# Performance work log

Measured on AMD Instinct MI355X. Metric: run time of the kernel, lower is better.

The kernel has to match this reference:

```python
import jax, jax.numpy as jnp
import numpy as np

N = 30000      # nodes
E = 300000     # edges (before self-loops)
G = 1024       # graphs
D_IN = 256     # embedding dim
HID = 256      # hidden dim
H = 8          # heads
C = HID // H   # per-head dim
VOCAB = 65


def setup_inputs() -> dict:
    key = jax.random.key(0)
    ks = jax.random.split(key, 32)
    inp = {
        "x_ids": jax.random.randint(ks[0], (N,), 0, VOCAB),
        "edge_index": jax.random.randint(ks[1], (2, E), 0, N),
        "batch_ids": (jnp.arange(N) * G) // N,  # sorted graph ids, every graph non-empty
        "emb": jax.random.normal(ks[2], (VOCAB, D_IN)) * 0.05,
        "fw": jax.random.normal(ks[3], (1, HID)) * 0.05,
        "fb": jnp.zeros((1,)),
    }
    k = 4
    for i, d_in in enumerate([D_IN, HID, HID, HID, HID], start=1):
        inp[f"W{i}"] = jax.random.normal(ks[k], (HID, d_in)) * (1.0 / np.sqrt(d_in)); k += 1
        inp[f"as{i}"] = jax.random.normal(ks[k], (H, C)) * 0.1; k += 1
        inp[f"ad{i}"] = jax.random.normal(ks[k], (H, C)) * 0.1; k += 1
        inp[f"b{i}"] = jnp.zeros((HID,))
    return inp


def _gat_conv(x, src, dst, W, a_src, a_dst, b):
    # x: [N, d_in] -> h: [N, H, C]
    h = (x @ W.T).reshape(N, H, C)
    e_src = jnp.einsum("nhc,hc->nh", h, a_src)  # [N, H]
    e_dst = jnp.einsum("nhc,hc->nh", h, a_dst)
    e = jax.nn.leaky_relu(e_src[src] + e_dst[dst], 0.2)  # [E', H]
    m = jax.ops.segment_max(e, dst, num_segments=N)      # segment softmax over incoming edges
    ex = jnp.exp(e - m[dst])
    s = jax.ops.segment_sum(ex, dst, num_segments=N)
    alpha = ex / (s[dst] + 1e-16)                        # [E', H]
    out = jax.ops.segment_sum(h[src] * alpha[:, :, None], dst, num_segments=N)
    return out.reshape(N, H * C) + b


def reference(x_ids, edge_index, batch_ids, emb,
              W1, as1, ad1, b1, W2, as2, ad2, b2, W3, as3, ad3, b3,
              W4, as4, ad4, b4, W5, as5, ad5, b5, fw, fb):
    # Embedding with max_norm=1: rescale looked-up rows whose L2 norm exceeds 1
    x = emb[x_ids]
    nrm = jnp.linalg.norm(x, axis=-1, keepdims=True)
    x = x * jnp.minimum(1.0, 1.0 / (nrm + 1e-12))
    # add self-loops once (PyG GATConv default)
    loop = jnp.arange(N)
    src = jnp.concatenate([edge_index[0], loop])
    dst = jnp.concatenate([edge_index[1], loop])
    x = jax.nn.relu(_gat_conv(x, src, dst, W1, as1, ad1, b1))
    x = jax.nn.relu(_gat_conv(x, src, dst, W2, as2, ad2, b2))
    x = jax.nn.relu(_gat_conv(x, src, dst, W3, as3, ad3, b3))
    x = jax.nn.relu(_gat_conv(x, src, dst, W4, as4, ad4, b4))
    x = jax.nn.relu(_gat_conv(x, src, dst, W5, as5, ad5, b5))
    pooled = jax.ops.segment_max(x, batch_ids, num_segments=G)  # [G, HID]
    return (pooled @ fw.T + fb).reshape(-1)  # [G]
```

## Files before the change

kernel.cpp:

```cpp
#include <hip/hip_runtime.h>
#include <float.h>
#include <math.h>

constexpr int NN  = 30000;
constexpr int EE  = 300000;
constexpr int GG  = 1024;
constexpr int HID = 256;
constexpr int NH  = 8;
constexpr int EP  = EE + NN;
constexpr int NP  = 30080;

typedef short bf16x8 __attribute__((ext_vector_type(8)));
typedef float f32x4 __attribute__((ext_vector_type(4)));

__device__ __forceinline__ void gload_lds16(const void* g, void* l) {
    __builtin_amdgcn_global_load_lds(
        (const __attribute__((address_space(1))) unsigned int*)g,
        (__attribute__((address_space(3))) unsigned int*)l, 16, 0, 0);
}

__device__ __forceinline__ void f2hilo(float x, unsigned short& h, unsigned short& l) {
    unsigned u = __float_as_uint(x);
    h = (unsigned short)(u >> 16);
    float hv = __uint_as_float(u & 0xFFFF0000u);
    float r = x - hv;
    unsigned v = __float_as_uint(r);
    unsigned rnd = ((v >> 16) & 1u) + 0x7FFFu;
    l = (unsigned short)((v + rnd) >> 16);
}

__device__ __forceinline__ float bf2f(unsigned short u) {
    return __uint_as_float(((unsigned)u) << 16);
}

__global__ void k_hist(const int* __restrict__ edst, int* __restrict__ cnt) {
    int i = blockIdx.x * blockDim.x + threadIdx.x;
    if (i >= EP) return;
    int d = (i < EE) ? edst[i] : (i - EE);
    atomicAdd(&cnt[d], 1);
}

__global__ void k_scan(const int* __restrict__ cnt, int* __restrict__ indptr) {
    __shared__ int wtot[16];
    __shared__ int carry_s;
    int tid = threadIdx.x;
    int lane = tid & 63, wid = tid >> 6;
    if (tid == 0) carry_s = 0;
    __syncthreads();
    for (int base = 0; base < NN; base += 1024) {
        int i = base + tid;
        int v = (i < NN) ? cnt[i] : 0;
        int incl = v;
        #pragma unroll
        for (int off = 1; off < 64; off <<= 1) {
            int t = __shfl_up(incl, off, 64);
            if (lane >= off) incl += t;
        }
        if (lane == 63) wtot[wid] = incl;
        __syncthreads();
        int wpre = 0;
        for (int w = 0; w < wid; ++w) wpre += wtot[w];
        int c = carry_s;
        if (i < NN) indptr[i] = c + wpre + incl - v;
        int tot = 0;
        for (int w = 0; w < 16; ++w) tot += wtot[w];
        __syncthreads();
        if (tid == 0) carry_s = c + tot;
        __syncthreads();
    }
    if (tid == 0) indptr[NN] = carry_s;
}

__global__ void k_fill(const int* __restrict__ esrc, const int* __restrict__ edst,
                       const int* __restrict__ indptr, int* __restrict__ cursor,
                       int* __restrict__ srcs) {
    int i = blockIdx.x * blockDim.x + threadIdx.x;
    if (i >= EP) return;
    int d, s;
    if (i < EE) { d = edst[i]; s = esrc[i]; } else { d = i - EE; s = i - EE; }
    int pos = indptr[d] + atomicAdd(&cursor[d], 1);
    srcs[pos] = s;
}

__global__ void k_sortseg(int* __restrict__ srcs, const int* __restrict__ indptr) {
    int node = blockIdx.x * blockDim.x + threadIdx.x;
    if (node >= NN) return;
    int b = indptr[node], e = indptr[node + 1];
    for (int i = b + 1; i < e; ++i) {
        int v = srcs[i];
        int j = i - 1;
        while (j >= b && srcs[j] > v) { srcs[j + 1] = srcs[j]; --j; }
        srcs[j + 1] = v;
    }
}

__global__ void k_starts(const int* __restrict__ batch, int* __restrict__ starts) {
    int i = blockIdx.x * blockDim.x + threadIdx.x;
    if (i >= NN) return;
    int b = batch[i];
    if (i == 0 || batch[i - 1] != b) starts[b] = i;
    if (i == NN - 1) starts[GG] = NN;
}

__global__ void k_wconv(const float* __restrict__ W1, const float* __restrict__ W2,
                        const float* __restrict__ W3, const float* __restrict__ W4,
                        const float* __restrict__ W5,
                        unsigned short* __restrict__ Whi, unsigned short* __restrict__ Wlo) {
    int i = blockIdx.x * blockDim.x + threadIdx.x;
    int l = blockIdx.y;
    const float* W = (l == 0) ? W1 : (l == 1) ? W2 : (l == 2) ? W3 : (l == 3) ? W4 : W5;
    unsigned short h, lo;
    f2hilo(W[i], h, lo);
    Whi[(size_t)l * 65536 + i] = h;
    Wlo[(size_t)l * 65536 + i] = lo;
}

__global__ void k_wtilde(const float* __restrict__ W, const float* __restrict__ as,
                         const float* __restrict__ ad,
                         unsigned short* __restrict__ Wthi, unsigned short* __restrict__ Wtlo) {
    int t = blockIdx.x;
    int k = threadIdx.x;
    int h = t >> 1, type = t & 1;
    const float* a = type ? ad : as;
    float v = 0.f;
    for (int c = 0; c < 32; ++c)
        v = fmaf(a[h * 32 + c], W[(size_t)(h * 32 + c) * HID + k], v);
    unsigned short hi, lo;
    f2hilo(v, hi, lo);
    Wthi[t * 256 + k] = hi;
    Wtlo[t * 256 + k] = lo;
}

__global__ void k_embed(const int* __restrict__ ids, const float* __restrict__ emb,
                        unsigned short* __restrict__ Phi, unsigned short* __restrict__ Plo) {
    int w = (blockIdx.x * blockDim.x + threadIdx.x) >> 6;
    if (w >= NN) return;
    int lane = threadIdx.x & 63;
    const float4 v = *(const float4*)(emb + (size_t)ids[w] * HID + lane * 4);
    float ss = v.x * v.x + v.y * v.y + v.z * v.z + v.w * v.w;
    #pragma unroll
    for (int off = 32; off >= 1; off >>= 1) ss += __shfl_xor(ss, off, 64);
    float nrm = sqrtf(ss);
    float sc = fminf(1.0f, 1.0f / (nrm + 1e-12f));
    float o[4] = {v.x * sc, v.y * sc, v.z * sc, v.w * sc};
    ushort4 hv, lv;
    f2hilo(o[0], hv.x, lv.x); f2hilo(o[1], hv.y, lv.y);
    f2hilo(o[2], hv.z, lv.z); f2hilo(o[3], hv.w, lv.w);
    *(ushort4*)(Phi + (size_t)w * HID + lane * 4) = hv;
    *(ushort4*)(Plo + (size_t)w * HID + lane * 4) = lv;
}

__global__ __launch_bounds__(256) void k_gemm(const unsigned short* __restrict__ Ahi,
                                              const unsigned short* __restrict__ Alo,
                                              const unsigned short* __restrict__ Bhi,
                                              const unsigned short* __restrict__ Blo,
                                              const unsigned short* __restrict__ Wthi,
                                              const unsigned short* __restrict__ Wtlo,
                                              float* __restrict__ O,
                                              float* __restrict__ es,
                                              float* __restrict__ ed, int M) {
    __shared__ unsigned short lds[4][128 * 64];
    const int tid = threadIdx.x;
    const int m0 = blockIdx.x * 128;
    const int n0 = blockIdx.y * 128;
    const int wid = tid >> 6, lane = tid & 63;
    const int wm = wid >> 1, wn = wid & 1;
    const int r16 = lane & 15, kq = lane >> 4;
    const bool doScore = (blockIdx.y == 1);

    f32x4 acc[4][4];
    f32x4 acc_s[4];
    #pragma unroll
    for (int i = 0; i < 4; ++i) {
        acc_s[i] = (f32x4){0.f, 0.f, 0.f, 0.f};
        #pragma unroll
        for (int j = 0; j < 4; ++j) acc[i][j] = (f32x4){0.f, 0.f, 0.f, 0.f};
    }

    for (int kt = 0; kt < 4; ++kt) {
        const int kk = kt * 64;
        #pragma unroll
        for (int rnd = 0; rnd < 4; ++rnd) {
            int q = rnd * 256 + tid;
            int row = q >> 3, c = q & 7;
            int sc = c ^ (row & 7);
            size_t goffA = (size_t)(m0 + row) * HID + kk + sc * 8;
            size_t goffB = (size_t)(n0 + row) * HID + kk + sc * 8;
            gload_lds16(Ahi + goffA, &lds[0][q * 8]);
            gload_lds16(Alo + goffA, &lds[1][q * 8]);
            gload_lds16(Bhi + goffB, &lds[2][q * 8]);
            gload_lds16(Blo + goffB, &lds[3][q * 8]);
        }
        __syncthreads();
        #pragma unroll
        for (int ks = 0; ks < 2; ++ks) {
            bf16x8 ah[4], al[4], bh[4], bl[4];
            #pragma unroll
            for (int f = 0; f < 4; ++f) {
                int rowa = wm * 64 + f * 16 + r16;
                int ca = (ks * 4 + kq) ^ (rowa & 7);
                int offa = rowa * 64 + ca * 8;
                ah[f] = *(const bf16x8*)&lds[0][offa];
                al[f] = *(const bf16x8*)&lds[1][offa];
                int rowb = wn * 64 + f * 16 + r16;
                int cb = (ks * 4 + kq) ^ (rowb & 7);
                int offb = rowb * 64 + cb * 8;
                bh[f] = *(const bf16x8*)&lds[2][offb];
                bl[f] = *(const bf16x8*)&lds[3][offb];
            }
            #pragma unroll
            for (int mi = 0; mi < 4; ++mi)
                #pragma unroll
                for (int ni = 0; ni < 4; ++ni) {
                    acc[mi][ni] = __builtin_amdgcn_mfma_f32_16x16x32_bf16(ah[mi], bh[ni], acc[mi][ni], 0, 0, 0);
                    acc[mi][ni] = __builtin_amdgcn_mfma_f32_16x16x32_bf16(ah[mi], bl[ni], acc[mi][ni], 0, 0, 0);
                    acc[mi][ni] = __builtin_amdgcn_mfma_f32_16x16x32_bf16(al[mi], bh[ni], acc[mi][ni], 0, 0, 0);
                }
            if (doScore && wn == ks) {
                const size_t wtoff = (size_t)r16 * HID + kk + ks * 32 + kq * 8;
                bf16x8 wth = *(const bf16x8*)(Wthi + wtoff);
                bf16x8 wtl = *(const bf16x8*)(Wtlo + wtoff);
                #pragma unroll
                for (int mi = 0; mi < 4; ++mi) {
                    acc_s[mi] = __builtin_amdgcn_mfma_f32_16x16x32_bf16(ah[mi], wth, acc_s[mi], 0, 0, 0);
                    acc_s[mi] = __builtin_amdgcn_mfma_f32_16x16x32_bf16(ah[mi], wtl, acc_s[mi], 0, 0, 0);
                    acc_s[mi] = __builtin_amdgcn_mfma_f32_16x16x32_bf16(al[mi], wth, acc_s[mi], 0, 0, 0);
                }
            }
        }
        __syncthreads();
    }
    #pragma unroll
    for (int mi = 0; mi < 4; ++mi) {
        #pragma unroll
        for (int q = 0; q < 4; ++q) {
            int row = m0 + wm * 64 + mi * 16 + kq * 4 + q;
            if (row < M) {
                #pragma unroll
                for (int ni = 0; ni < 4; ++ni)
                    O[(size_t)row * HID + n0 + wn * 64 + ni * 16 + r16] = acc[mi][ni][q];
            }
        }
    }
    if (doScore) {
        float* sl = (float*)&lds[0][0];
        if (wn == 1) {
            #pragma unroll
            for (int mi = 0; mi < 4; ++mi)
                *(f32x4*)&sl[((wm * 4 + mi) * 64 + lane) * 4] = acc_s[mi];
        }
        __syncthreads();
        if (wn == 0) {
            #pragma unroll
            for (int mi = 0; mi < 4; ++mi) {
                f32x4 o = *(const f32x4*)&sl[((wm * 4 + mi) * 64 + lane) * 4];
                o += acc_s[mi];
                int h = r16 >> 1;
                #pragma unroll
                for (int q = 0; q < 4; ++q) {
                    int row = m0 + wm * 64 + mi * 16 + kq * 4 + q;
                    if (row < M) {
                        if ((r16 & 1) == 0) es[row * NH + h] = o[q];
                        else               ed[row * NH + h] = o[q];
                    }
                }
            }
        }
    }
}

__global__ __launch_bounds__(256) void k_aggregate(const float* __restrict__ H,
                                                   const float* __restrict__ es,
                                                   const float* __restrict__ ed,
                                                   const int* __restrict__ indptr,
                                                   const int* __restrict__ srcs,
                                                   const float* __restrict__ bias,
                                                   unsigned short* __restrict__ Phi,
                                                   unsigned short* __restrict__ Plo) {
    int node = (blockIdx.x * blockDim.x + threadIdx.x) >> 6;
    if (node >= NN) return;
    int lane = threadIdx.x & 63;
    int head = lane >> 3;
    int b0 = indptr[node], e0 = indptr[node + 1];
    float edv = ed[node * NH + head];
    float4 a[4];
    float s[4];
    #pragma unroll
    for (int u = 0; u < 4; ++u) { a[u] = (float4){0.f, 0.f, 0.f, 0.f}; s[u] = 0.f; }
    int j = b0;
    for (; j + 3 < e0; j += 4) {
        #pragma unroll
        for (int u = 0; u < 4; ++u) {
            int x = srcs[j + u];
            float e = es[x * NH + head] + edv;
            e = (e > 0.f) ? e : 0.2f * e;
            float4 hv = *(const float4*)(H + (size_t)x * HID + lane * 4);
            float w = expf(e);
            s[u] += w;
            a[u].x = fmaf(w, hv.x, a[u].x); a[u].y = fmaf(w, hv.y, a[u].y);
            a[u].z = fmaf(w, hv.z, a[u].z); a[u].w = fmaf(w, hv.w, a[u].w);
        }
    }
    for (; j < e0; ++j) {
        int x = srcs[j];
        float e = es[x * NH + head] + edv;
        e = (e > 0.f) ? e : 0.2f * e;
        float4 hv = *(const float4*)(H + (size_t)x * HID + lane * 4);
        float w = expf(e);
        s[0] += w;
        a[0].x = fmaf(w, hv.x, a[0].x); a[0].y = fmaf(w, hv.y, a[0].y);
        a[0].z = fmaf(w, hv.z, a[0].z); a[0].w = fmaf(w, hv.w, a[0].w);
    }
    float sum = (s[0] + s[1]) + (s[2] + s[3]);
    float ax = (a[0].x + a[1].x) + (a[2].x + a[3].x);
    float ay = (a[0].y + a[1].y) + (a[2].y + a[3].y);
    float az = (a[0].z + a[1].z) + (a[2].z + a[3].z);
    float aw = (a[0].w + a[1].w) + (a[2].w + a[3].w);
    float inv = 1.f / (sum + 1e-16f);
    float4 bv = *(const float4*)(bias + lane * 4);
    float o[4];
    o[0] = fmaxf(fmaf(ax, inv, bv.x), 0.f);
    o[1] = fmaxf(fmaf(ay, inv, bv.y), 0.f);
    o[2] = fmaxf(fmaf(az, inv, bv.z), 0.f);
    o[3] = fmaxf(fmaf(aw, inv, bv.w), 0.f);
    ushort4 hv, lv;
    f2hilo(o[0], hv.x, lv.x); f2hilo(o[1], hv.y, lv.y);
    f2hilo(o[2], hv.z, lv.z); f2hilo(o[3], hv.w, lv.w);
    *(ushort4*)(Phi + (size_t)node * HID + lane * 4) = hv;
    *(ushort4*)(Plo + (size_t)node * HID + lane * 4) = lv;
}

__global__ void k_pool(const unsigned short* __restrict__ Phi,
                       const unsigned short* __restrict__ Plo,
                       const int* __restrict__ starts,
                       const float* __restrict__ fw, const float* __restrict__ fb,
                       float* __restrict__ out) {
    int g = (blockIdx.x * blockDim.x + threadIdx.x) >> 6;
    if (g >= GG) return;
    int lane = threadIdx.x & 63;
    int s = starts[g], e = starts[g + 1];
    float mx0 = -FLT_MAX, mx1 = -FLT_MAX, mx2 = -FLT_MAX, mx3 = -FLT_MAX;
    for (int n = s; n < e; ++n) {
        ushort4 hv = *(const ushort4*)(Phi + (size_t)n * HID + lane * 4);
        ushort4 lv = *(const ushort4*)(Plo + (size_t)n * HID + lane * 4);
        mx0 = fmaxf(mx0, bf2f(hv.x) + bf2f(lv.x));
        mx1 = fmaxf(mx1, bf2f(hv.y) + bf2f(lv.y));
        mx2 = fmaxf(mx2, bf2f(hv.z) + bf2f(lv.z));
        mx3 = fmaxf(mx3, bf2f(hv.w) + bf2f(lv.w));
    }
    float4 w = *(const float4*)(fw + lane * 4);
    float t = mx0 * w.x + mx1 * w.y + mx2 * w.z + mx3 * w.w;
    #pragma unroll
    for (int off = 32; off >= 1; off >>= 1) t += __shfl_xor(t, off, 64);
    if (lane == 0) out[g] = t + fb[0];
}

extern "C" void kernel_launch(void* const* d_in, const int* in_sizes, int n_in,
                              void* d_out, int out_size, void* d_ws, size_t ws_size,
                              hipStream_t stream) {
    const int* x_ids = (const int*)d_in[0];
    const int* eidx  = (const int*)d_in[1];
    const int* batch = (const int*)d_in[2];
    const float* emb = (const float*)d_in[3];
    const float* fw  = (const float*)d_in[4];
    const float* fb  = (const float*)d_in[5];
    const float* Wl[5], *asl[5], *adl[5], *bl[5];
    for (int l = 0; l < 5; ++l) {
        Wl[l]  = (const float*)d_in[6 + 4 * l];
        asl[l] = (const float*)d_in[7 + 4 * l];
        adl[l] = (const float*)d_in[8 + 4 * l];
        bl[l]  = (const float*)d_in[9 + 4 * l];
    }

    char* ws = (char*)d_ws;
    size_t off = 0;
    auto alloc = [&](size_t bytes) {
        void* p = ws + off;
        off = (off + bytes + 255) & ~(size_t)255;
        return p;
    };
    unsigned short* Phi  = (unsigned short*)alloc((size_t)NP * HID * 2);
    unsigned short* Plo  = (unsigned short*)alloc((size_t)NP * HID * 2);
    float* Q     = (float*)alloc((size_t)NN * HID * 4);
    unsigned short* Whi  = (unsigned short*)alloc((size_t)5 * HID * HID * 2);
    unsigned short* Wlo  = (unsigned short*)alloc((size_t)5 * HID * HID * 2);
    unsigned short* Wthi = (unsigned short*)alloc((size_t)5 * 16 * HID * 2);
    unsigned short* Wtlo = (unsigned short*)alloc((size_t)5 * 16 * HID * 2);
    float* es    = (float*)alloc((size_t)NN * NH * 4);
    float* ed    = (float*)alloc((size_t)NN * NH * 4);
    int* cnt     = (int*)alloc((size_t)NN * 4);
    int* cursor  = (int*)alloc((size_t)NN * 4);
    int* indptr  = (int*)alloc((size_t)(NN + 1) * 4);
    int* srcs    = (int*)alloc((size_t)EP * 4);
    int* starts  = (int*)alloc((size_t)(GG + 1) * 4);
    (void)ws_size; (void)in_sizes; (void)n_in; (void)out_size;

    hipMemsetAsync(cnt, 0, (size_t)NN * 4, stream);
    hipMemsetAsync(cursor, 0, (size_t)NN * 4, stream);

    k_hist<<<(EP + 255) / 256, 256, 0, stream>>>(eidx + EE, cnt);
    k_scan<<<1, 1024, 0, stream>>>(cnt, indptr);
    k_fill<<<(EP + 255) / 256, 256, 0, stream>>>(eidx, eidx + EE, indptr, cursor, srcs);
    k_sortseg<<<(NN + 255) / 256, 256, 0, stream>>>(srcs, indptr);
    k_starts<<<(NN + 255) / 256, 256, 0, stream>>>(batch, starts);
    k_wconv<<<dim3(HID * HID / 256, 5), 256, 0, stream>>>(Wl[0], Wl[1], Wl[2], Wl[3], Wl[4], Whi, Wlo);
    for (int l = 0; l < 5; ++l)
        k_wtilde<<<16, 256, 0, stream>>>(Wl[l], asl[l], adl[l],
                                         Wthi + (size_t)l * 16 * HID,
                                         Wtlo + (size_t)l * 16 * HID);
    k_embed<<<NN / 4, 256, 0, stream>>>(x_ids, emb, Phi, Plo);

    for (int l = 0; l < 5; ++l) {
        dim3 gg(NP / 128, HID / 128);
        k_gemm<<<gg, 256, 0, stream>>>(Phi, Plo,
                                       Whi + (size_t)l * HID * HID,
                                       Wlo + (size_t)l * HID * HID,
                                       Wthi + (size_t)l * 16 * HID,
                                       Wtlo + (size_t)l * 16 * HID,
                                       Q, es, ed, NN);
        k_aggregate<<<NN / 4, 256, 0, stream>>>(Q, es, ed, indptr, srcs, bl[l], Phi, Plo);
    }
    k_pool<<<GG / 4, 256, 0, stream>>>(Phi, Plo, starts, fw, fb, (float*)d_out);
}
```

Measured before the change: 527.8 us.

## Parallelize CSR scan, halve GEMM K-tile, split score MFMAs, deepen aggregation prefetch

Replaces the single-block serial prefix scan with a three-kernel block-parallel scan (block sums, offsets, per-block scan). The GEMM K-tile shrinks from 64 to 32 with a new LDS swizzle, which halves LDS use for higher occupancy but doubles the number of barriers. The attention-score MFMAs are now split across the two N-warps by M fragment, which removes the LDS reduction and its extra barrier. The aggregation loop is unrolled to 8 edges with all index, score and feature loads issued before the math, to get more gathers in flight at the cost of more registers.

```diff
diff --git a/kernel.cpp b/kernel.cpp
--- a/kernel.cpp
+++ b/kernel.cpp
@@ -9,6 +9,7 @@
 constexpr int NH  = 8;
 constexpr int EP  = EE + NN;
 constexpr int NP  = 30080;
+constexpr int NB  = (NN + 255) / 256;
 
 typedef short bf16x8 __attribute__((ext_vector_type(8)));
 typedef float f32x4 __attribute__((ext_vector_type(4)));
@@ -40,35 +41,53 @@
     atomicAdd(&cnt[d], 1);
 }
 
-__global__ void k_scan(const int* __restrict__ cnt, int* __restrict__ indptr) {
-    __shared__ int wtot[16];
-    __shared__ int carry_s;
-    int tid = threadIdx.x;
-    int lane = tid & 63, wid = tid >> 6;
-    if (tid == 0) carry_s = 0;
+__global__ void k_scan1(const int* __restrict__ cnt, int* __restrict__ bsum) {
+    int tid = threadIdx.x, lane = tid & 63, wid = tid >> 6;
+    int i = blockIdx.x * 256 + tid;
+    int v = (i < NN) ? cnt[i] : 0;
+    #pragma unroll
+    for (int off = 32; off >= 1; off >>= 1) v += __shfl_xor(v, off, 64);
+    __shared__ int ws[4];
+    if (lane == 0) ws[wid] = v;
     __syncthreads();
-    for (int base = 0; base < NN; base += 1024) {
-        int i = base + tid;
-        int v = (i < NN) ? cnt[i] : 0;
-        int incl = v;
-        #pragma unroll
-        for (int off = 1; off < 64; off <<= 1) {
-            int t = __shfl_up(incl, off, 64);
-            if (lane >= off) incl += t;
-        }
-        if (lane == 63) wtot[wid] = incl;
-        __syncthreads();
-        int wpre = 0;
-        for (int w = 0; w < wid; ++w) wpre += wtot[w];
-        int c = carry_s;
-        if (i < NN) indptr[i] = c + wpre + incl - v;
-        int tot = 0;
-        for (int w = 0; w < 16; ++w) tot += wtot[w];
-        __syncthreads();
-        if (tid == 0) carry_s = c + tot;
-        __syncthreads();
-    }
-    if (tid == 0) indptr[NN] = carry_s;
+    if (tid == 0) bsum[blockIdx.x] = ws[0] + ws[1] + ws[2] + ws[3];
+}
+
+__global__ void k_scan2(const int* __restrict__ bsum, int* __restrict__ boff,
+                        int* __restrict__ indptr) {
+    int tid = threadIdx.x, lane = tid & 63, wid = tid >> 6;
+    int v = (tid < NB) ? bsum[tid] : 0;
+    int incl = v;
+    #pragma unroll
+    for (int off = 1; off < 64; off <<= 1) {
+        int t = __shfl_up(incl, off, 64);
+        if (lane >= off) incl += t;
+    }
+    __shared__ int ws[2];
+    if (lane == 63) ws[wid] = incl;
+    __syncthreads();
+    int pre = (wid == 1) ? ws[0] : 0;
+    if (tid < NB) boff[tid] = pre + incl - v;
+    if (tid == 0) indptr[NN] = ws[0] + ws[1];
+}
+
+__global__ void k_scan3(const int* __restrict__ cnt, const int* __restrict__ boff,
+                        int* __restrict__ indptr) {
+    int tid = threadIdx.x, lane = tid & 63, wid = tid >> 6;
+    int i = blockIdx.x * 256 + tid;
+    int v = (i < NN) ? cnt[i] : 0;
+    int incl = v;
+    #pragma unroll
+    for (int off = 1; off < 64; off <<= 1) {
+        int t = __shfl_up(incl, off, 64);
+        if (lane >= off) incl += t;
+    }
+    __shared__ int ws[4];
+    if (lane == 63) ws[wid] = incl;
+    __syncthreads();
+    int pre = 0;
+    for (int w = 0; w < wid; ++w) pre += ws[w];
+    if (i < NN) indptr[i] = boff[blockIdx.x] + pre + incl - v;
 }
 
 __global__ void k_fill(const int* __restrict__ esrc, const int* __restrict__ edst,
@@ -159,7 +178,7 @@
                                               float* __restrict__ O,
                                               float* __restrict__ es,
                                               float* __restrict__ ed, int M) {
-    __shared__ unsigned short lds[4][128 * 64];
+    __shared__ unsigned short lds[4][128 * 32];
     const int tid = threadIdx.x;
     const int m0 = blockIdx.x * 128;
     const int n0 = blockIdx.y * 128;
@@ -169,63 +188,61 @@
     const bool doScore = (blockIdx.y == 1);
 
     f32x4 acc[4][4];
-    f32x4 acc_s[4];
-    #pragma unroll
-    for (int i = 0; i < 4; ++i) {
-        acc_s[i] = (f32x4){0.f, 0.f, 0.f, 0.f};
+    f32x4 acc_s[2];
+    acc_s[0] = (f32x4){0.f, 0.f, 0.f, 0.f};
+    acc_s[1] = (f32x4){0.f, 0.f, 0.f, 0.f};
+    #pragma unroll
+    for (int i = 0; i < 4; ++i)
         #pragma unroll
         for (int j = 0; j < 4; ++j) acc[i][j] = (f32x4){0.f, 0.f, 0.f, 0.f};
-    }
-
-    for (int kt = 0; kt < 4; ++kt) {
-        const int kk = kt * 64;
-        #pragma unroll
-        for (int rnd = 0; rnd < 4; ++rnd) {
+
+    for (int kt = 0; kt < 8; ++kt) {
+        const int kk = kt * 32;
+        #pragma unroll
+        for (int rnd = 0; rnd < 2; ++rnd) {
             int q = rnd * 256 + tid;
-            int row = q >> 3, c = q & 7;
-            int sc = c ^ (row & 7);
-            size_t goffA = (size_t)(m0 + row) * HID + kk + sc * 8;
-            size_t goffB = (size_t)(n0 + row) * HID + kk + sc * 8;
+            int row = q >> 2, c = q & 3;
+            int l = ((c + 4 - ((row >> 2) & 3)) & 3) ^ (row & 3);
+            size_t goffA = (size_t)(m0 + row) * HID + kk + l * 8;
+            size_t goffB = (size_t)(n0 + row) * HID + kk + l * 8;
             gload_lds16(Ahi + goffA, &lds[0][q * 8]);
             gload_lds16(Alo + goffA, &lds[1][q * 8]);
             gload_lds16(Bhi + goffB, &lds[2][q * 8]);
             gload_lds16(Blo + goffB, &lds[3][q * 8]);
         }
         __syncthreads();
-        #pragma unroll
-        for (int ks = 0; ks < 2; ++ks) {
-            bf16x8 ah[4], al[4], bh[4], bl[4];
+        bf16x8 ah[4], al[4], bh[4], bl[4];
+        #pragma unroll
+        for (int f = 0; f < 4; ++f) {
+            int rowa = wm * 64 + f * 16 + r16;
+            int pa = ((kq ^ (rowa & 3)) + ((rowa >> 2) & 3)) & 3;
+            int offa = rowa * 32 + pa * 8;
+            ah[f] = *(const bf16x8*)&lds[0][offa];
+            al[f] = *(const bf16x8*)&lds[1][offa];
+            int rowb = wn * 64 + f * 16 + r16;
+            int pb = ((kq ^ (rowb & 3)) + ((rowb >> 2) & 3)) & 3;
+            int offb = rowb * 32 + pb * 8;
+            bh[f] = *(const bf16x8*)&lds[2][offb];
+            bl[f] = *(const bf16x8*)&lds[3][offb];
+        }
+        #pragma unroll
+        for (int mi = 0; mi < 4; ++mi)
             #pragma unroll
-            for (int f = 0; f < 4; ++f) {
-                int rowa = wm * 64 + f * 16 + r16;
-                int ca = (ks * 4 + kq) ^ (rowa & 7);
-                int offa = rowa * 64 + ca * 8;
-                ah[f] = *(const bf16x8*)&lds[0][offa];
-                al[f] = *(const bf16x8*)&lds[1][offa];
-                int rowb = wn * 64 + f * 16 + r16;
-                int cb = (ks * 4 + kq) ^ (rowb & 7);
-                int offb = rowb * 64 + cb * 8;
-                bh[f] = *(const bf16x8*)&lds[2][offb];
-                bl[f] = *(const bf16x8*)&lds[3][offb];
+            for (int ni = 0; ni < 4; ++ni) {
+                acc[mi][ni] = __builtin_amdgcn_mfma_f32_16x16x32_bf16(ah[mi], bh[ni], acc[mi][ni], 0, 0, 0);
+                acc[mi][ni] = __builtin_amdgcn_mfma_f32_16x16x32_bf16(ah[mi], bl[ni], acc[mi][ni], 0, 0, 0);
+                acc[mi][ni] = __builtin_amdgcn_mfma_f32_16x16x32_bf16(al[mi], bh[ni], acc[mi][ni], 0, 0, 0);
             }
+        if (doScore) {
+            const size_t wtoff = (size_t)r16 * HID + kk + kq * 8;
+            bf16x8 wth = *(const bf16x8*)(Wthi + wtoff);
+            bf16x8 wtl = *(const bf16x8*)(Wtlo + wtoff);
             #pragma unroll
-            for (int mi = 0; mi < 4; ++mi)
-                #pragma unroll
-                for (int ni = 0; ni < 4; ++ni) {
-                    acc[mi][ni] = __builtin_amdgcn_mfma_f32_16x16x32_bf16(ah[mi], bh[ni], acc[mi][ni], 0, 0, 0);
-                    acc[mi][ni] = __builtin_amdgcn_mfma_f32_16x16x32_bf16(ah[mi], bl[ni], acc[mi][ni], 0, 0, 0);
-                    acc[mi][ni] = __builtin_amdgcn_mfma_f32_16x16x32_bf16(al[mi], bh[ni], acc[mi][ni], 0, 0, 0);
-                }
-            if (doScore && wn == ks) {
-                const size_t wtoff = (size_t)r16 * HID + kk + ks * 32 + kq * 8;
-                bf16x8 wth = *(const bf16x8*)(Wthi + wtoff);
-                bf16x8 wtl = *(const bf16x8*)(Wtlo + wtoff);
-                #pragma unroll
-                for (int mi = 0; mi < 4; ++mi) {
-                    acc_s[mi] = __builtin_amdgcn_mfma_f32_16x16x32_bf16(ah[mi], wth, acc_s[mi], 0, 0, 0);
-                    acc_s[mi] = __builtin_amdgcn_mfma_f32_16x16x32_bf16(ah[mi], wtl, acc_s[mi], 0, 0, 0);
-                    acc_s[mi] = __builtin_amdgcn_mfma_f32_16x16x32_bf16(al[mi], wth, acc_s[mi], 0, 0, 0);
-                }
+            for (int ml = 0; ml < 2; ++ml) {
+                int mi = wn * 2 + ml;
+                acc_s[ml] = __builtin_amdgcn_mfma_f32_16x16x32_bf16(ah[mi], wth, acc_s[ml], 0, 0, 0);
+                acc_s[ml] = __builtin_amdgcn_mfma_f32_16x16x32_bf16(ah[mi], wtl, acc_s[ml], 0, 0, 0);
+                acc_s[ml] = __builtin_amdgcn_mfma_f32_16x16x32_bf16(al[mi], wth, acc_s[ml], 0, 0, 0);
             }
         }
         __syncthreads();
@@ -243,26 +260,16 @@
         }
     }
     if (doScore) {
-        float* sl = (float*)&lds[0][0];
-        if (wn == 1) {
+        int h = r16 >> 1;
+        #pragma unroll
+        for (int ml = 0; ml < 2; ++ml) {
+            int mi = wn * 2 + ml;
             #pragma unroll
-            for (int mi = 0; mi < 4; ++mi)
-                *(f32x4*)&sl[((wm * 4 + mi) * 64 + lane) * 4] = acc_s[mi];
-        }
-        __syncthreads();
-        if (wn == 0) {
-            #pragma unroll
-            for (int mi = 0; mi < 4; ++mi) {
-                f32x4 o = *(const f32x4*)&sl[((wm * 4 + mi) * 64 + lane) * 4];
-                o += acc_s[mi];
-                int h = r16 >> 1;
-                #pragma unroll
-                for (int q = 0; q < 4; ++q) {
-                    int row = m0 + wm * 64 + mi * 16 + kq * 4 + q;
-                    if (row < M) {
-                        if ((r16 & 1) == 0) es[row * NH + h] = o[q];
-                        else               ed[row * NH + h] = o[q];
-                    }
+            for (int q = 0; q < 4; ++q) {
+                int row = m0 + wm * 64 + mi * 16 + kq * 4 + q;
+                if (row < M) {
+                    if ((r16 & 1) == 0) es[row * NH + h] = acc_s[ml][q];
+                    else               ed[row * NH + h] = acc_s[ml][q];
                 }
             }
         }
@@ -288,17 +295,26 @@
     #pragma unroll
     for (int u = 0; u < 4; ++u) { a[u] = (float4){0.f, 0.f, 0.f, 0.f}; s[u] = 0.f; }
     int j = b0;
-    for (; j + 3 < e0; j += 4) {
-        #pragma unroll
-        for (int u = 0; u < 4; ++u) {
-            int x = srcs[j + u];
-            float e = es[x * NH + head] + edv;
+    for (; j + 7 < e0; j += 8) {
+        int x[8];
+        float ev[8];
+        float4 hv[8];
+        #pragma unroll
+        for (int u = 0; u < 8; ++u) x[u] = srcs[j + u];
+        #pragma unroll
+        for (int u = 0; u < 8; ++u) ev[u] = es[x[u] * NH + head];
+        #pragma unroll
+        for (int u = 0; u < 8; ++u) hv[u] = *(const float4*)(H + (size_t)x[u] * HID + lane * 4);
+        #pragma unroll
+        for (int u = 0; u < 8; ++u) {
+            float e = ev[u] + edv;
             e = (e > 0.f) ? e : 0.2f * e;
-            float4 hv = *(const float4*)(H + (size_t)x * HID + lane * 4);
             float w = expf(e);
-            s[u] += w;
-            a[u].x = fmaf(w, hv.x, a[u].x); a[u].y = fmaf(w, hv.y, a[u].y);
-            a[u].z = fmaf(w, hv.z, a[u].z); a[u].w = fmaf(w, hv.w, a[u].w);
+            s[u & 3] += w;
+            a[u & 3].x = fmaf(w, hv[u].x, a[u & 3].x);
+            a[u & 3].y = fmaf(w, hv[u].y, a[u & 3].y);
+            a[u & 3].z = fmaf(w, hv[u].z, a[u & 3].z);
+            a[u & 3].w = fmaf(w, hv[u].w, a[u & 3].w);
         }
     }
     for (; j < e0; ++j) {
@@ -323,11 +339,11 @@
     o[1] = fmaxf(fmaf(ay, inv, bv.y), 0.f);
     o[2] = fmaxf(fmaf(az, inv, bv.z), 0.f);
     o[3] = fmaxf(fmaf(aw, inv, bv.w), 0.f);
-    ushort4 hv, lv;
-    f2hilo(o[0], hv.x, lv.x); f2hilo(o[1], hv.y, lv.y);
-    f2hilo(o[2], hv.z, lv.z); f2hilo(o[3], hv.w, lv.w);
-    *(ushort4*)(Phi + (size_t)node * HID + lane * 4) = hv;
-    *(ushort4*)(Plo + (size_t)node * HID + lane * 4) = lv;
+    ushort4 hv2, lv2;
+    f2hilo(o[0], hv2.x, lv2.x); f2hilo(o[1], hv2.y, lv2.y);
+    f2hilo(o[2], hv2.z, lv2.z); f2hilo(o[3], hv2.w, lv2.w);
+    *(ushort4*)(Phi + (size_t)node * HID + lane * 4) = hv2;
+    *(ushort4*)(Plo + (size_t)node * HID + lane * 4) = lv2;
 }
 
 __global__ void k_pool(const unsigned short* __restrict__ Phi,
@@ -392,6 +408,8 @@
     int* cursor  = (int*)alloc((size_t)NN * 4);
     int* indptr  = (int*)alloc((size_t)(NN + 1) * 4);
     int* srcs    = (int*)alloc((size_t)EP * 4);
+    int* bsum    = (int*)alloc((size_t)NB * 4);
+    int* boff    = (int*)alloc((size_t)NB * 4);
     int* starts  = (int*)alloc((size_t)(GG + 1) * 4);
     (void)ws_size; (void)in_sizes; (void)n_in; (void)out_size;
 
@@ -399,7 +417,9 @@
     hipMemsetAsync(cursor, 0, (size_t)NN * 4, stream);
 
     k_hist<<<(EP + 255) / 256, 256, 0, stream>>>(eidx + EE, cnt);
-    k_scan<<<1, 1024, 0, stream>>>(cnt, indptr);
+    k_scan1<<<NB, 256, 0, stream>>>(cnt, bsum);
+    k_scan2<<<1, 128, 0, stream>>>(bsum, boff, indptr);
+    k_scan3<<<NB, 256, 0, stream>>>(cnt, boff, indptr);
     k_fill<<<(EP + 255) / 256, 256, 0, stream>>>(eidx, eidx + EE, indptr, cursor, srcs);
     k_sortseg<<<(NN + 255) / 256, 256, 0, stream>>>(srcs, indptr);
     k_starts<<<(NN + 255) / 256, 256, 0, stream>>>(batch, starts);
```

Result: slower. 615.7 us (+16.7%).
